# Kernel tuning notes

Hardware: AMD Instinct MI355X
Metric: run time of the kernel (lower is better)

## Reference

```python
import jax, jax.numpy as jnp
import numpy as np

D_MODEL = 512
NUM_HEADS = 8
D_K = D_MODEL // NUM_HEADS
MAX_REL = 64
B, L = 8, 512


def setup_inputs() -> dict:
    key = jax.random.key(0)
    ks = jax.random.split(key, 11)
    d = D_MODEL
    s = 1.0 / np.sqrt(d)
    return {
        "x": jax.random.normal(ks[0], (B, L, d), dtype=jnp.float32),
        "Wq": jax.random.normal(ks[1], (d, d), dtype=jnp.float32) * s,
        "bq": jnp.zeros((d,), dtype=jnp.float32),
        "Wk": jax.random.normal(ks[2], (d, d), dtype=jnp.float32) * s,
        "bk": jnp.zeros((d,), dtype=jnp.float32),
        "Wv": jax.random.normal(ks[3], (d, d), dtype=jnp.float32) * s,
        "bv": jnp.zeros((d,), dtype=jnp.float32),
        "Wo": jax.random.normal(ks[4], (d, d), dtype=jnp.float32) * s,
        "bo": jnp.zeros((d,), dtype=jnp.float32),
        "rel_k": jax.random.normal(ks[5], (2 * MAX_REL + 1, NUM_HEADS, D_K), dtype=jnp.float32),
        "rel_v": jax.random.normal(ks[6], (2 * MAX_REL + 1, NUM_HEADS, D_K), dtype=jnp.float32),
    }


def reference(x, Wq, bq, Wk, bk, Wv, bv, Wo, bo, rel_k, rel_v):
    Bsz, Ls, Dm = x.shape
    H, dk = NUM_HEADS, D_K

    def heads(y):  # [B,L,D] -> [B,H,L,dk]
        return y.reshape(Bsz, Ls, H, dk).transpose(0, 2, 1, 3)

    Q = heads(x @ Wq + bq)
    K = heads(x @ Wk + bk)
    V = heads(x @ Wv + bv)  # computed as in original (its svrel branch is discarded)

    content = jnp.einsum('bhld,bhmd->bhlm', Q, K)

    pos = jnp.arange(Ls)
    rel_idx = jnp.clip(pos[:, None] - pos[None, :], -MAX_REL, MAX_REL) + MAX_REL  # [L,L]
    relK = rel_k[rel_idx]  # [L,L,H,dk]
    relV = rel_v[rel_idx]  # [L,L,H,dk]

    rel_scores = jnp.einsum('bhld,lmhd->bhlm', Q, relK)
    attn = jax.nn.softmax((content + rel_scores) / jnp.sqrt(jnp.float32(dk)), axis=-1)

    # NOTE: the original computes svrel = attn @ V but the line `attn_output + svrel`
    # discards its result; the output uses ONLY the relative-value term. Replicated.
    out = jnp.einsum('bhlm,lmhd->bhld', attn, relV)  # [B,H,L,dk]
    out = out.transpose(0, 2, 1, 3).reshape(Bsz, Ls, Dm)
    return out @ Wo + bo
```

## Files before the change

kernel.cpp:

```cpp
#include <hip/hip_runtime.h>

#define NB 8
#define NL 512
#define ND 512
#define NH 8
#define NDK 64
#define NR 129
#define NTOK 4096
#define RPAD 132
#define PST 136

typedef unsigned short u16;
typedef unsigned int u32;
typedef __attribute__((ext_vector_type(4))) float f32x4;
typedef __attribute__((ext_vector_type(8))) u16 u16x8;
typedef __attribute__((ext_vector_type(8))) __bf16 bf16x8;

__device__ __forceinline__ u16 f2bf(float f) {
  u32 u = __float_as_uint(f);
  u += 0x7FFFu + ((u >> 16) & 1u);
  return (u16)(u >> 16);
}
__device__ __forceinline__ float bf2f(u16 s) {
  return __uint_as_float(((u32)s) << 16);
}

__global__ __launch_bounds__(256) void convert_pack(
    const float* __restrict__ x, const float* __restrict__ Wq,
    const float* __restrict__ Wk, const float* __restrict__ Wo,
    const float* __restrict__ bq, const float* __restrict__ bk,
    const float* __restrict__ rel_k, u16* __restrict__ xb,
    u16* __restrict__ Wqkt, u16* __restrict__ Wot, float* __restrict__ bqk,
    u16* __restrict__ relkb) {
  const int bx = blockIdx.x, tid = threadIdx.x;
  if (bx < 256) {
    const int tg = bx * 256 + tid;
#pragma unroll
    for (int it = 0; it < 4; ++it) {
      const int s = tg + it * 65536;
      f32x4 a = *(const f32x4*)&x[s * 8];
      f32x4 b = *(const f32x4*)&x[s * 8 + 4];
      u16x8 o;
#pragma unroll
      for (int e = 0; e < 4; ++e) { o[e] = f2bf(a[e]); o[4 + e] = f2bf(b[e]); }
      *(u16x8*)&xb[s * 8] = o;
    }
  } else if (bx < 260) {
    const int t = (bx - 256) * 256 + tid;
    bqk[t] = (t < 512) ? bq[t] : bk[t - 512];
    for (int i = t; i < NR * NH * NDK; i += 1024) {
      int j = i >> 9, rest = i & 511;
      int h = rest >> 6, d = rest & 63;
      relkb[(h * NR + j) * NDK + d] = f2bf(rel_k[i]);
    }
  } else {
    __shared__ u16 T[64 * 65];
    const int wi = bx - 260;
    const int mi = wi >> 6, ti = wi & 63;
    const int r0 = (ti >> 3) * 64, c0 = (ti & 7) * 64;
    const float* W = (mi == 0) ? Wq : (mi == 1) ? Wk : Wo;
#pragma unroll
    for (int it = 0; it < 4; ++it) {
      const int s = tid + it * 256;
      const int row = s >> 4, c4 = s & 15;
      f32x4 v = *(const f32x4*)&W[(r0 + row) * ND + c0 + c4 * 4];
#pragma unroll
      for (int e = 0; e < 4; ++e) T[(c4 * 4 + e) * 65 + row] = f2bf(v[e]);
    }
    __syncthreads();
#pragma unroll
    for (int it = 0; it < 2; ++it) {
      const int s = tid + it * 256;
      const int oc = s >> 3, oseg = (s & 7) * 8;
      u16x8 o;
#pragma unroll
      for (int e = 0; e < 8; ++e) o[e] = T[oc * 65 + oseg + e];
      if (mi == 2)
        *(u16x8*)&Wot[(c0 + oc) * ND + r0 + oseg] = o;
      else
        *(u16x8*)&Wqkt[(mi * ND + c0 + oc) * ND + r0 + oseg] = o;
    }
  }
}

template <int MODE>
__global__ __launch_bounds__(256) void gemm_xw(const u16* __restrict__ A,
                                               const u16* __restrict__ Wt,
                                               const float* __restrict__ bias,
                                               void* __restrict__ outp) {
  constexpr int AST = 40;
  __shared__ alignas(16) u16 As[64 * AST];
  __shared__ alignas(16) u16 Bs[64 * AST];
  const int tid = threadIdx.x;
  const int lane = tid & 63, wave = tid >> 6;
  const int wm = wave >> 1, wn = wave & 1;
  const int m0 = blockIdx.x * 64, n0 = blockIdx.y * 64;
  const int kq = (lane >> 4) << 3, rl = lane & 15;
  const int srow = tid >> 2, sseg = (tid & 3) << 3;
  const f32x4 zero = {0.f, 0.f, 0.f, 0.f};
  f32x4 acc[2][2];
#pragma unroll
  for (int i = 0; i < 2; ++i)
#pragma unroll
    for (int j = 0; j < 2; ++j) acc[i][j] = zero;

  for (int k0 = 0; k0 < 512; k0 += 32) {
    __syncthreads();
    *(u16x8*)&As[srow * AST + sseg] =
        *(const u16x8*)&A[(m0 + srow) * 512 + k0 + sseg];
    *(u16x8*)&Bs[srow * AST + sseg] =
        *(const u16x8*)&Wt[(n0 + srow) * 512 + k0 + sseg];
    __syncthreads();
    bf16x8 af[2], bg[2];
#pragma unroll
    for (int f = 0; f < 2; ++f)
      af[f] = *(const bf16x8*)&As[(wm * 32 + f * 16 + rl) * AST + kq];
#pragma unroll
    for (int f = 0; f < 2; ++f)
      bg[f] = *(const bf16x8*)&Bs[(wn * 32 + f * 16 + rl) * AST + kq];
#pragma unroll
    for (int i = 0; i < 2; ++i)
#pragma unroll
      for (int j = 0; j < 2; ++j)
        acc[i][j] = __builtin_amdgcn_mfma_f32_16x16x32_bf16(af[i], bg[j],
                                                            acc[i][j], 0, 0, 0);
  }

  const int rb = (lane >> 4) << 2;
#pragma unroll
  for (int i = 0; i < 2; ++i) {
#pragma unroll
    for (int j = 0; j < 2; ++j) {
      const int c = n0 + wn * 32 + j * 16 + rl;
      const float bv = bias[c];
#pragma unroll
      for (int r = 0; r < 4; ++r) {
        const int row = m0 + wm * 32 + i * 16 + rb + r;
        const float v = acc[i][j][r] + bv;
        if (MODE == 0) {
          const int is_k = c >> 9, nn = c & 511;
          const int b = row >> 9, l = row & 511, h = nn >> 6, d = nn & 63;
          ((u16*)outp)[(size_t)is_k * (NB * NH * NL * NDK) +
                       ((size_t)(b * NH + h) * NL + l) * NDK + d] = f2bf(v);
        } else {
          ((float*)outp)[(size_t)row * ND + c] = v;
        }
      }
    }
  }
}

__global__ __launch_bounds__(256) void gemm_qkt(const u16* __restrict__ Qb,
                                                const u16* __restrict__ Kb,
                                                float* __restrict__ S) {
  constexpr int AST = 40;
  __shared__ alignas(16) u16 As[128 * AST];
  __shared__ alignas(16) u16 Bs[128 * AST];
  const int tid = threadIdx.x;
  const int lane = tid & 63, wave = tid >> 6;
  const int wm = wave >> 1, wn = wave & 1;
  const int bh = blockIdx.z;
  const u16* Aq = Qb + (size_t)bh * NL * NDK;
  const u16* Bk = Kb + (size_t)bh * NL * NDK;
  float* Sout = S + (size_t)bh * NL * NL;
  const int m0 = blockIdx.x * 128, n0 = blockIdx.y * 128;
  const int kq = (lane >> 4) << 3, rl = lane & 15;
  const f32x4 zero = {0.f, 0.f, 0.f, 0.f};
  f32x4 acc[4][4];
#pragma unroll
  for (int i = 0; i < 4; ++i)
#pragma unroll
    for (int j = 0; j < 4; ++j) acc[i][j] = zero;

  for (int k0 = 0; k0 < 64; k0 += 32) {
    __syncthreads();
#pragma unroll
    for (int r = 0; r < 2; ++r) {
      int idx = r * 256 + tid;
      int row = idx >> 2, seg = (idx & 3) << 3;
      *(u16x8*)&As[row * AST + seg] =
          *(const u16x8*)&Aq[(m0 + row) * NDK + k0 + seg];
      *(u16x8*)&Bs[row * AST + seg] =
          *(const u16x8*)&Bk[(n0 + row) * NDK + k0 + seg];
    }
    __syncthreads();
    bf16x8 af[4], bg[4];
#pragma unroll
    for (int f = 0; f < 4; ++f)
      af[f] = *(const bf16x8*)&As[(wm * 64 + f * 16 + rl) * AST + kq];
#pragma unroll
    for (int f = 0; f < 4; ++f)
      bg[f] = *(const bf16x8*)&Bs[(wn * 64 + f * 16 + rl) * AST + kq];
#pragma unroll
    for (int i = 0; i < 4; ++i)
#pragma unroll
      for (int j = 0; j < 4; ++j)
        acc[i][j] = __builtin_amdgcn_mfma_f32_16x16x32_bf16(af[i], bg[j],
                                                            acc[i][j], 0, 0, 0);
  }

  const int rb = (lane >> 4) << 2;
#pragma unroll
  for (int i = 0; i < 4; ++i)
#pragma unroll
    for (int j = 0; j < 4; ++j) {
      const int c = n0 + wn * 64 + j * 16 + rl;
#pragma unroll
      for (int r = 0; r < 4; ++r) {
        const int row = m0 + wm * 64 + i * 16 + rb + r;
        Sout[(size_t)row * NL + c] = acc[i][j][r];
      }
    }
}

__global__ __launch_bounds__(256) void rel_scores_k(const u16* __restrict__ Qb,
                                                    const u16* __restrict__ relkb,
                                                    float* __restrict__ R) {
  __shared__ float relk_f[NR * NDK];
  const int tid = threadIdx.x;
  const int bh = blockIdx.y, h = bh & 7, l0 = blockIdx.x * 64;
  for (int i = tid; i < NR * NDK; i += 256)
    relk_f[i] = bf2f(relkb[h * NR * NDK + i]);
  __syncthreads();
  const int row = tid >> 2, jq = tid & 3;
  const u16* qrow = Qb + ((size_t)bh * NL + l0 + row) * NDK;
  float q[64];
#pragma unroll
  for (int v = 0; v < 8; ++v) {
    u16x8 t = *(const u16x8*)&qrow[v * 8];
#pragma unroll
    for (int e = 0; e < 8; ++e) q[v * 8 + e] = bf2f(t[e]);
  }
  float* Rrow = R + ((size_t)bh * NL + l0 + row) * RPAD;
  const int j0 = jq * 33, j1 = (j0 + 33 < NR) ? j0 + 33 : NR;
#pragma unroll 1
  for (int j = j0; j < j1; ++j) {
    float a0 = 0.f, a1 = 0.f, a2 = 0.f, a3 = 0.f;
    const float* rk = &relk_f[j * 64];
#pragma unroll
    for (int e = 0; e < 16; ++e) {
      a0 += q[e] * rk[e];
      a1 += q[16 + e] * rk[16 + e];
      a2 += q[32 + e] * rk[32 + e];
      a3 += q[48 + e] * rk[48 + e];
    }
    Rrow[j] = (a0 + a1) + (a2 + a3);
  }
}

__global__ __launch_bounds__(256) void softagg(const float* __restrict__ S,
                                               const float* __restrict__ R,
                                               const float* __restrict__ rel_v,
                                               u16* __restrict__ OH) {
  __shared__ alignas(16) u16 relvT[64 * PST];
  __shared__ alignas(16) u16 P_s[4][16 * PST];
  __shared__ float t0s[4][16], t1s[4][16];
  const int tid = threadIdx.x;
  const int lane = tid & 63, wave = tid >> 6;
  const int chunk = blockIdx.x, bh = blockIdx.y;
  const int h = bh & 7, b = bh >> 3;

#pragma unroll 4
  for (int jb = 0; jb < 128; jb += 4) {
    const int j = jb + (tid >> 6), d = tid & 63;
    relvT[d * PST + j] = f2bf(rel_v[j * (NH * NDK) + h * NDK + d]);
  }
  if ((tid & 3) == 0) {
    const u16x8 z = {0, 0, 0, 0, 0, 0, 0, 0};
    *(u16x8*)&relvT[(tid >> 2) * PST + 128] = z;
  }
  {
    const u16x8 z = {0, 0, 0, 0, 0, 0, 0, 0};
    for (int i = tid; i < 1088; i += 256) *(u16x8*)&((u16*)P_s)[i * 8] = z;
  }
  __syncthreads();

  u16* P_w = P_s[wave];
#pragma unroll 2
  for (int r = 0; r < 16; ++r) {
    const int l = chunk * 64 + wave * 16 + r;
    const float* Srow = S + ((size_t)bh * NL + l) * NL;
    const float* Rrow = R + ((size_t)bh * NL + l) * RPAD;
    const f32x4 s0 = *(const f32x4*)(Srow + lane * 8);
    const f32x4 s1 = *(const f32x4*)(Srow + lane * 8 + 4);
    float sv[8];
#pragma unroll
    for (int t = 0; t < 4; ++t) { sv[t] = s0[t]; sv[4 + t] = s1[t]; }

    float lg[8], mx = -1e30f;
#pragma unroll
    for (int t = 0; t < 8; ++t) {
      const int m = lane * 8 + t;
      const int dd = l - m;
      const int j = (dd <= -64) ? 0 : ((dd >= 64) ? 128 : dd + 64);
      lg[t] = (sv[t] + Rrow[j]) * 0.125f;
      mx = fmaxf(mx, lg[t]);
    }
#pragma unroll
    for (int off = 32; off >= 1; off >>= 1) mx = fmaxf(mx, __shfl_xor(mx, off, 64));
    float p[8], sum = 0.f;
#pragma unroll
    for (int t = 0; t < 8; ++t) { p[t] = __expf(lg[t] - mx); sum += p[t]; }
#pragma unroll
    for (int off = 32; off >= 1; off >>= 1) sum += __shfl_xor(sum, off, 64);
    const float inv = 1.f / sum;

    float t0 = 0.f, t1 = 0.f;
#pragma unroll
    for (int t = 0; t < 8; ++t) {
      const int m = lane * 8 + t;
      const int dd = l - m;
      const float a = p[t] * inv;
      if (dd >= 64) t1 += a;
      else if (dd <= -64) t0 += a;
      else P_w[r * PST + 64 + dd] = f2bf(a);
    }
#pragma unroll
    for (int off = 32; off >= 1; off >>= 1) {
      t0 += __shfl_xor(t0, off, 64);
      t1 += __shfl_xor(t1, off, 64);
    }
    if (lane == 0) { t0s[wave][r] = t0; t1s[wave][r] = t1; }
  }

  const int rl = lane & 15, kq = (lane >> 4) << 3;
  const f32x4 zero = {0.f, 0.f, 0.f, 0.f};
  f32x4 acc[4] = {zero, zero, zero, zero};
#pragma unroll
  for (int ks = 0; ks < 4; ++ks) {
    bf16x8 af = *(const bf16x8*)&P_w[rl * PST + ks * 32 + kq];
#pragma unroll
    for (int nt = 0; nt < 4; ++nt) {
      bf16x8 bg = *(const bf16x8*)&relvT[(nt * 16 + rl) * PST + ks * 32 + kq];
      acc[nt] = __builtin_amdgcn_mfma_f32_16x16x32_bf16(af, bg, acc[nt], 0, 0, 0);
    }
  }

#pragma unroll
  for (int nt = 0; nt < 4; ++nt) {
    const int d = nt * 16 + rl;
    const float rv0 = rel_v[0 * (NH * NDK) + h * NDK + d];
    const float rv128 = rel_v[128 * (NH * NDK) + h * NDK + d];
#pragma unroll
    for (int reg = 0; reg < 4; ++reg) {
      const int rloc = (lane >> 4) * 4 + reg;
      const int l_out = chunk * 64 + wave * 16 + rloc;
      const float v = acc[nt][reg] + t0s[wave][rloc] * rv0 + t1s[wave][rloc] * rv128;
      OH[((size_t)b * NL + l_out) * ND + h * NDK + d] = f2bf(v);
    }
  }
}

extern "C" void kernel_launch(void* const* d_in, const int* in_sizes, int n_in,
                              void* d_out, int out_size, void* d_ws,
                              size_t ws_size, hipStream_t stream) {
  const float* x = (const float*)d_in[0];
  const float* Wq = (const float*)d_in[1];
  const float* bq = (const float*)d_in[2];
  const float* Wk = (const float*)d_in[3];
  const float* bk = (const float*)d_in[4];
  const float* Wo = (const float*)d_in[7];
  const float* bo = (const float*)d_in[8];
  const float* rel_k = (const float*)d_in[9];
  const float* rel_v = (const float*)d_in[10];

  char* ws = (char*)d_ws;
  size_t off = 0;
  auto alloc = [&](size_t bytes) {
    void* p = ws + off;
    off = (off + bytes + 255) & ~(size_t)255;
    return p;
  };
  u16* xb = (u16*)alloc((size_t)NTOK * ND * 2);
  u16* Wqkt = (u16*)alloc((size_t)2 * ND * ND * 2);
  u16* Wot = (u16*)alloc((size_t)ND * ND * 2);
  float* bqk = (float*)alloc((size_t)2 * ND * 4);
  u16* relkb = (u16*)alloc((size_t)NH * NR * NDK * 2);
  u16* QKb = (u16*)alloc((size_t)2 * NB * NH * NL * NDK * 2);
  float* Sbuf = (float*)alloc((size_t)NB * NH * NL * NL * 4);
  float* Rbuf = (float*)alloc((size_t)NB * NH * NL * RPAD * 4);
  u16* OH = (u16*)alloc((size_t)NTOK * ND * 2);
  u16* Qb = QKb;
  u16* Kb = QKb + (size_t)NB * NH * NL * NDK;

  convert_pack<<<452, 256, 0, stream>>>(x, Wq, Wk, Wo, bq, bk, rel_k, xb, Wqkt,
                                        Wot, bqk, relkb);
  gemm_xw<0><<<dim3(64, 16), 256, 0, stream>>>(xb, Wqkt, bqk, QKb);
  gemm_qkt<<<dim3(4, 4, 64), 256, 0, stream>>>(Qb, Kb, Sbuf);
  rel_scores_k<<<dim3(8, 64), 256, 0, stream>>>(Qb, relkb, Rbuf);
  softagg<<<dim3(8, 64), 256, 0, stream>>>(Sbuf, Rbuf, rel_v, OH);
  gemm_xw<1><<<dim3(64, 8), 256, 0, stream>>>(OH, Wot, bo, d_out);
}
```

Baseline: 194.6 us.

## Use MFMA for relative-key scores and store QK^T scores in bf16

Replaces the scalar-FMA relative score kernel with a bf16 MFMA kernel that computes Q·rel_k for 128 rows against 144 padded relative positions per block. The content score buffer S is now written and read as bf16 instead of fp32, which halves the traffic of the largest intermediate (64x512x512). In exchange, S is stored at reduced precision before the softmax, and the padded rel_k rows 129-143 are never written, so that buffer area is left uninitialized. Those padded columns are only read by the MFMA for R columns that softagg ignores.

```diff
diff --git a/kernel.cpp b/kernel.cpp
--- a/kernel.cpp
+++ b/kernel.cpp
@@ -6,8 +6,8 @@
 #define NH 8
 #define NDK 64
 #define NR 129
+#define NRP 144
 #define NTOK 4096
-#define RPAD 132
 #define PST 136
 
 typedef unsigned short u16;
@@ -51,7 +51,7 @@
     for (int i = t; i < NR * NH * NDK; i += 1024) {
       int j = i >> 9, rest = i & 511;
       int h = rest >> 6, d = rest & 63;
-      relkb[(h * NR + j) * NDK + d] = f2bf(rel_k[i]);
+      relkb[((size_t)h * NRP + j) * NDK + d] = f2bf(rel_k[i]);
     }
   } else {
     __shared__ u16 T[64 * 65];
@@ -152,7 +152,7 @@
 
 __global__ __launch_bounds__(256) void gemm_qkt(const u16* __restrict__ Qb,
                                                 const u16* __restrict__ Kb,
-                                                float* __restrict__ S) {
+                                                u16* __restrict__ S) {
   constexpr int AST = 40;
   __shared__ alignas(16) u16 As[128 * AST];
   __shared__ alignas(16) u16 Bs[128 * AST];
@@ -162,7 +162,7 @@
   const int bh = blockIdx.z;
   const u16* Aq = Qb + (size_t)bh * NL * NDK;
   const u16* Bk = Kb + (size_t)bh * NL * NDK;
-  float* Sout = S + (size_t)bh * NL * NL;
+  u16* Sout = S + (size_t)bh * NL * NL;
   const int m0 = blockIdx.x * 128, n0 = blockIdx.y * 128;
   const int kq = (lane >> 4) << 3, rl = lane & 15;
   const f32x4 zero = {0.f, 0.f, 0.f, 0.f};
@@ -208,47 +208,74 @@
 #pragma unroll
       for (int r = 0; r < 4; ++r) {
         const int row = m0 + wm * 64 + i * 16 + rb + r;
-        Sout[(size_t)row * NL + c] = acc[i][j][r];
+        Sout[(size_t)row * NL + c] = f2bf(acc[i][j][r]);
       }
     }
 }
 
-__global__ __launch_bounds__(256) void rel_scores_k(const u16* __restrict__ Qb,
-                                                    const u16* __restrict__ relkb,
-                                                    float* __restrict__ R) {
-  __shared__ float relk_f[NR * NDK];
+__global__ __launch_bounds__(256) void rel_scores_mfma(
+    const u16* __restrict__ Qb, const u16* __restrict__ relkb,
+    float* __restrict__ R) {
+  constexpr int AST = 72;
+  __shared__ alignas(16) u16 Qs[128 * AST];
+  __shared__ alignas(16) u16 Bs[NRP * AST];
   const int tid = threadIdx.x;
-  const int bh = blockIdx.y, h = bh & 7, l0 = blockIdx.x * 64;
-  for (int i = tid; i < NR * NDK; i += 256)
-    relk_f[i] = bf2f(relkb[h * NR * NDK + i]);
+  const int lane = tid & 63, wave = tid >> 6;
+  const int bh = blockIdx.y, h = bh & 7;
+  const int m0 = blockIdx.x * 128;
+
+  for (int i = tid; i < 128 * 8; i += 256) {
+    int row = i >> 3, seg = (i & 7) << 3;
+    *(u16x8*)&Qs[row * AST + seg] =
+        *(const u16x8*)&Qb[((size_t)bh * NL + m0 + row) * NDK + seg];
+  }
+  for (int i = tid; i < NRP * 8; i += 256) {
+    int row = i >> 3, seg = (i & 7) << 3;
+    *(u16x8*)&Bs[row * AST + seg] =
+        *(const u16x8*)&relkb[((size_t)h * NRP + row) * NDK + seg];
+  }
   __syncthreads();
-  const int row = tid >> 2, jq = tid & 3;
-  const u16* qrow = Qb + ((size_t)bh * NL + l0 + row) * NDK;
-  float q[64];
-#pragma unroll
-  for (int v = 0; v < 8; ++v) {
-    u16x8 t = *(const u16x8*)&qrow[v * 8];
-#pragma unroll
-    for (int e = 0; e < 8; ++e) q[v * 8 + e] = bf2f(t[e]);
-  }
-  float* Rrow = R + ((size_t)bh * NL + l0 + row) * RPAD;
-  const int j0 = jq * 33, j1 = (j0 + 33 < NR) ? j0 + 33 : NR;
-#pragma unroll 1
-  for (int j = j0; j < j1; ++j) {
-    float a0 = 0.f, a1 = 0.f, a2 = 0.f, a3 = 0.f;
-    const float* rk = &relk_f[j * 64];
-#pragma unroll
-    for (int e = 0; e < 16; ++e) {
-      a0 += q[e] * rk[e];
-      a1 += q[16 + e] * rk[16 + e];
-      a2 += q[32 + e] * rk[32 + e];
-      a3 += q[48 + e] * rk[48 + e];
-    }
-    Rrow[j] = (a0 + a1) + (a2 + a3);
-  }
-}
-
-__global__ __launch_bounds__(256) void softagg(const float* __restrict__ S,
+
+  const int rl = lane & 15, kq = (lane >> 4) << 3;
+  const f32x4 zero = {0.f, 0.f, 0.f, 0.f};
+  f32x4 acc[2][9];
+#pragma unroll
+  for (int i = 0; i < 2; ++i)
+#pragma unroll
+    for (int j = 0; j < 9; ++j) acc[i][j] = zero;
+
+#pragma unroll
+  for (int ks = 0; ks < 2; ++ks) {
+    bf16x8 af[2], bg[9];
+#pragma unroll
+    for (int i = 0; i < 2; ++i)
+      af[i] = *(const bf16x8*)&Qs[(wave * 32 + i * 16 + rl) * AST + ks * 32 + kq];
+#pragma unroll
+    for (int j = 0; j < 9; ++j)
+      bg[j] = *(const bf16x8*)&Bs[(j * 16 + rl) * AST + ks * 32 + kq];
+#pragma unroll
+    for (int i = 0; i < 2; ++i)
+#pragma unroll
+      for (int j = 0; j < 9; ++j)
+        acc[i][j] = __builtin_amdgcn_mfma_f32_16x16x32_bf16(af[i], bg[j],
+                                                            acc[i][j], 0, 0, 0);
+  }
+
+  const int rb = (lane >> 4) << 2;
+#pragma unroll
+  for (int i = 0; i < 2; ++i)
+#pragma unroll
+    for (int j = 0; j < 9; ++j) {
+      const int c = j * 16 + rl;
+#pragma unroll
+      for (int r = 0; r < 4; ++r) {
+        const int row = m0 + wave * 32 + i * 16 + rb + r;
+        R[((size_t)bh * NL + row) * NRP + c] = acc[i][j][r];
+      }
+    }
+}
+
+__global__ __launch_bounds__(256) void softagg(const u16* __restrict__ S,
                                                const float* __restrict__ R,
                                                const float* __restrict__ rel_v,
                                                u16* __restrict__ OH) {
@@ -279,13 +306,12 @@
 #pragma unroll 2
   for (int r = 0; r < 16; ++r) {
     const int l = chunk * 64 + wave * 16 + r;
-    const float* Srow = S + ((size_t)bh * NL + l) * NL;
-    const float* Rrow = R + ((size_t)bh * NL + l) * RPAD;
-    const f32x4 s0 = *(const f32x4*)(Srow + lane * 8);
-    const f32x4 s1 = *(const f32x4*)(Srow + lane * 8 + 4);
+    const u16* Srow = S + ((size_t)bh * NL + l) * NL;
+    const float* Rrow = R + ((size_t)bh * NL + l) * NRP;
+    const u16x8 sraw = *(const u16x8*)(Srow + lane * 8);
     float sv[8];
 #pragma unroll
-    for (int t = 0; t < 4; ++t) { sv[t] = s0[t]; sv[4 + t] = s1[t]; }
+    for (int t = 0; t < 8; ++t) sv[t] = bf2f(sraw[t]);
 
     float lg[8], mx = -1e30f;
 #pragma unroll
@@ -375,10 +401,10 @@
   u16* Wqkt = (u16*)alloc((size_t)2 * ND * ND * 2);
   u16* Wot = (u16*)alloc((size_t)ND * ND * 2);
   float* bqk = (float*)alloc((size_t)2 * ND * 4);
-  u16* relkb = (u16*)alloc((size_t)NH * NR * NDK * 2);
+  u16* relkb = (u16*)alloc((size_t)NH * NRP * NDK * 2);
   u16* QKb = (u16*)alloc((size_t)2 * NB * NH * NL * NDK * 2);
-  float* Sbuf = (float*)alloc((size_t)NB * NH * NL * NL * 4);
-  float* Rbuf = (float*)alloc((size_t)NB * NH * NL * RPAD * 4);
+  u16* Sbuf = (u16*)alloc((size_t)NB * NH * NL * NL * 2);
+  float* Rbuf = (float*)alloc((size_t)NB * NH * NL * NRP * 4);
   u16* OH = (u16*)alloc((size_t)NTOK * ND * 2);
   u16* Qb = QKb;
   u16* Kb = QKb + (size_t)NB * NH * NL * NDK;
@@ -387,7 +413,7 @@
                                         Wot, bqk, relkb);
   gemm_xw<0><<<dim3(64, 16), 256, 0, stream>>>(xb, Wqkt, bqk, QKb);
   gemm_qkt<<<dim3(4, 4, 64), 256, 0, stream>>>(Qb, Kb, Sbuf);
-  rel_scores_k<<<dim3(8, 64), 256, 0, stream>>>(Qb, relkb, Rbuf);
+  rel_scores_mfma<<<dim3(4, 64), 256, 0, stream>>>(Qb, relkb, Rbuf);
   softagg<<<dim3(8, 64), 256, 0, stream>>>(Sbuf, Rbuf, rel_v, OH);
   gemm_xw<1><<<dim3(64, 8), 256, 0, stream>>>(OH, Wot, bo, d_out);
 }
```

Result: faster. 160.6 us (-17.4%).
